# Kernel optimization log

Measured on AMD Instinct MI355X. Metric: run time of the kernel, lower is better.

Reference implementation:

```python
import jax, jax.numpy as jnp
import numpy as np

N = 100000
E = 1000000
IN_C = 128
HID = 128
HEADS = 4
DH = HID // HEADS
L = 2
RWSE_DIM = 16
WALK_LEN = 16
NPAIRS = 200000
EPS = 1e-5


def setup_inputs() -> dict:
    key = jax.random.key(0)
    ks = jax.random.split(key, 20)
    x = jax.random.normal(ks[0], (N, IN_C), dtype=jnp.float32)
    rw_diag = jax.random.uniform(ks[1], (N, WALK_LEN), dtype=jnp.float32)
    edge_index = jax.random.randint(ks[2], (2, E), 0, N, dtype=jnp.int32)
    src = jax.random.randint(ks[3], (NPAIRS,), 0, N, dtype=jnp.int32)
    dst = jax.random.randint(ks[4], (NPAIRS,), 0, N, dtype=jnp.int32)
    s = 0.05
    W_rwse = jax.random.normal(ks[5], (WALK_LEN, RWSE_DIM), dtype=jnp.float32) * s
    b_rwse = jnp.zeros((RWSE_DIM,), dtype=jnp.float32)
    W_in = jax.random.normal(ks[6], (IN_C + RWSE_DIM, HID), dtype=jnp.float32) * s
    b_in = jnp.zeros((HID,), dtype=jnp.float32)
    Wq = jax.random.normal(ks[7], (L, HID, HID), dtype=jnp.float32) * s
    bq = jnp.zeros((L, HID), dtype=jnp.float32)
    Wk = jax.random.normal(ks[8], (L, HID, HID), dtype=jnp.float32) * s
    bk = jnp.zeros((L, HID), dtype=jnp.float32)
    Wv = jax.random.normal(ks[9], (L, HID, HID), dtype=jnp.float32) * s
    bv = jnp.zeros((L, HID), dtype=jnp.float32)
    Ws = jax.random.normal(ks[10], (L, HID, HID), dtype=jnp.float32) * s
    bs = jnp.zeros((L, HID), dtype=jnp.float32)
    ln_g = jnp.ones((L, HID), dtype=jnp.float32)
    ln_b = jnp.zeros((L, HID), dtype=jnp.float32)
    return {"x": x, "rw_diag": rw_diag, "edge_index": edge_index, "src": src,
            "dst": dst, "W_rwse": W_rwse, "b_rwse": b_rwse, "W_in": W_in,
            "b_in": b_in, "Wq": Wq, "bq": bq, "Wk": Wk, "bk": bk, "Wv": Wv,
            "bv": bv, "Ws": Ws, "bs": bs, "ln_g": ln_g, "ln_b": ln_b}


def reference(x, rw_diag, edge_index, src, dst, W_rwse, b_rwse, W_in, b_in,
              Wq, bq, Wk, bk, Wv, bv, Ws, bs, ln_g, ln_b):
    row = edge_index[0]  # message source j
    col = edge_index[1]  # message target i
    # RWSE projection + input projection
    pe = rw_diag @ W_rwse + b_rwse                      # [N, rwse_dim]
    h = jnp.concatenate([x, pe], axis=-1) @ W_in + b_in  # [N, HID]
    scale = 1.0 / jnp.sqrt(jnp.float32(DH))
    for l in range(L):
        q = (h @ Wq[l] + bq[l]).reshape(N, HEADS, DH)
        k = (h @ Wk[l] + bk[l]).reshape(N, HEADS, DH)
        v = (h @ Wv[l] + bv[l]).reshape(N, HEADS, DH)
        # per-edge attention scores (gather)
        score = jnp.einsum('ehd,ehd->eh', q[col], k[row]) * scale  # [E, H]
        # segment softmax over incoming edges of each target node
        m = jax.ops.segment_max(score, col, num_segments=N)   # [N, H]
        ex = jnp.exp(score - m[col])
        z = jax.ops.segment_sum(ex, col, num_segments=N)      # [N, H]
        alpha = ex / z[col]                                   # [E, H]
        agg = jax.ops.segment_sum(alpha[:, :, None] * v[row], col,
                                  num_segments=N).reshape(N, HID)
        conv = agg + h @ Ws[l] + bs[l]  # root/skip linear (PyG lin_skip)
        # residual + LayerNorm + ReLU
        y = h + conv
        mu = jnp.mean(y, axis=-1, keepdims=True)
        var = jnp.mean(jnp.square(y - mu), axis=-1, keepdims=True)
        h = jax.nn.relu(ln_g[l] * (y - mu) / jnp.sqrt(var + EPS) + ln_b[l])
    logits = jnp.sum(h[src] * h[dst], axis=-1)  # [NPAIRS]
    return jax.nn.sigmoid(logits)
```

## Files before the change

### kernel.cpp

```cpp
#include <hip/hip_runtime.h>
#include <hip/hip_bf16.h>
#include <cstdint>


#define NN      100000
#define EE      1000000
#define RWSEC   16
#define WALKC   16
#define NPAIRSC 200000
#define BSH     9
#define BKT     ((NN + 511) >> BSH)

typedef unsigned int       u32;
typedef unsigned short     u16;
typedef unsigned char      u8;
typedef __attribute__((ext_vector_type(8))) short    short8;
typedef __attribute__((ext_vector_type(4))) float    f32x4;
typedef __attribute__((ext_vector_type(2))) _Float16 h2;

__device__ __forceinline__ float bflo(u32 u){ return __uint_as_float(u << 16); }
__device__ __forceinline__ float bfhi(u32 u){ return __uint_as_float(u & 0xffff0000u); }
__device__ __forceinline__ u16 f2bf(float f){
    u32 u = __float_as_uint(f);
    u += 0x7fffu + ((u >> 16) & 1u);
    return (u16)(u >> 16);
}
__device__ __forceinline__ u32 pack2(float a, float b){
    return (u32)f2bf(a) | ((u32)f2bf(b) << 16);
}

#if defined(__has_builtin)
#if __has_builtin(__builtin_amdgcn_cvt_pk_f32_fp8) && __has_builtin(__builtin_amdgcn_cvt_pk_fp8_f32)
#define HWFP8 1
#endif
#if __has_builtin(__builtin_amdgcn_sdot4)
#define USE_SDOT4 1
#endif
#if __has_builtin(__builtin_amdgcn_cvt_pk_f16_fp8)
#define HWF16FP8 1
#endif
#endif

#ifndef HWFP8
__device__ __forceinline__ float fp8dec1(u32 b){
    u32 s = (b >> 7) & 1u, e = (b >> 3) & 15u, m = b & 7u;
    float mag = e ? __uint_as_float(((e + 120u) << 23) | (m << 20))
                  : (float)m * 0.001953125f;
    return s ? -mag : mag;
}
__device__ __forceinline__ u32 fp8enc1(float f){
    u32 u = __float_as_uint(f); u32 s = (u >> 31) << 7; float a = fabsf(f);
    if (a >= 448.f) return s | 0x7Eu;
    u32 ua = __float_as_uint(a);
    ua += 0x7FFFFu + ((ua >> 20) & 1u);
    int e = (int)(ua >> 23) - 127 + 7;
    if (e <= 0){ int m = (int)rintf(a * 512.f); return s | (u32)m; }
    u32 m = (ua >> 20) & 7u;
    return s | ((u32)e << 3) | m;
}
#endif

__device__ __forceinline__ void fp8x4_dec(u32 w4, float& f0, float& f1, float& f2, float& f3){
#ifdef HWFP8
    auto lo = __builtin_amdgcn_cvt_pk_f32_fp8((int)w4, false);
    auto hi = __builtin_amdgcn_cvt_pk_f32_fp8((int)w4, true);
    f0 = lo[0]; f1 = lo[1]; f2 = hi[0]; f3 = hi[1];
#else
    f0 = fp8dec1(w4 & 255u); f1 = fp8dec1((w4 >> 8) & 255u);
    f2 = fp8dec1((w4 >> 16) & 255u); f3 = fp8dec1(w4 >> 24);
#endif
}
__device__ __forceinline__ u32 fp8x4_enc(float f0, float f1, float f2, float f3){
#ifdef HWFP8
    u32 t = (u32)__builtin_amdgcn_cvt_pk_fp8_f32(f0, f1, 0, false);
    return (u32)__builtin_amdgcn_cvt_pk_fp8_f32(f2, f3, (int)t, true);
#else
    return fp8enc1(f0) | (fp8enc1(f1) << 8) | (fp8enc1(f2) << 16) | (fp8enc1(f3) << 24);
#endif
}
__device__ __forceinline__ void fp8x4_to_h2(u32 w, h2& lo, h2& hi){
#ifdef HWF16FP8
    lo = __builtin_bit_cast(h2, __builtin_amdgcn_cvt_pk_f16_fp8((int)w, false));
    hi = __builtin_bit_cast(h2, __builtin_amdgcn_cvt_pk_f16_fp8((int)w, true));
#else
    float f0, f1, f2, f3;
    fp8x4_dec(w, f0, f1, f2, f3);
    lo = __builtin_bit_cast(h2, __builtin_amdgcn_cvt_pkrtz(f0, f1));
    hi = __builtin_bit_cast(h2, __builtin_amdgcn_cvt_pkrtz(f2, f3));
#endif
}

#define QSCALE    48.0f
#define DESCALE2  1.10693e-4f

__device__ __forceinline__ int i8q(float f){
    float c = fminf(fmaxf(f * QSCALE, -127.f), 127.f);
    return (int)rintf(c);
}
__device__ __forceinline__ u32 i8x4_enc(float f0, float f1, float f2, float f3){
    return (u32)(i8q(f0) & 255) | ((u32)(i8q(f1) & 255) << 8)
         | ((u32)(i8q(f2) & 255) << 16) | ((u32)(i8q(f3) & 255) << 24);
}
__device__ __forceinline__ float sb(u32 w, int i){
    return (float)(int)(signed char)((w >> (i * 8)) & 255u);
}

__global__ __launch_bounds__(256) void winprep_kernel(const float* __restrict__ Win,
                                                      u16* __restrict__ Winb){
    int t = blockIdx.x * 256 + threadIdx.x;
    if (t >= 8 * 5 * 64) return;
    int lane = t & 63, fi = t >> 6;
    int nt = fi / 5, kk = fi - nt * 5;
    int col = nt * 16 + (lane & 15);
    int k0  = kk * 32 + (lane >> 4) * 8;
    u16* dst = Winb + (size_t)fi * 512 + lane * 8;
    #pragma unroll
    for (int e = 0; e < 8; ++e){
        int k = k0 + e;
        dst[e] = (k < 144) ? f2bf(Win[(size_t)k * 128 + col]) : (u16)0;
    }
}

__global__ __launch_bounds__(512, 8) void inproj_mfma(const float* __restrict__ x,
        const float* __restrict__ rw, const float* __restrict__ Wr,
        const float* __restrict__ br,
        const u16* __restrict__ Winb, const float* __restrict__ bin,
        u16* __restrict__ hb){
    __shared__ u16   hs[64 * 168];
    __shared__ float rws[64 * 16];
    int tid = threadIdx.x;
    int n0  = blockIdx.x * 64;

    #pragma unroll
    for (int i = 0; i < 4; ++i){
        int g   = i * 512 + tid;
        int row = g >> 5, c4 = g & 31;
        float4 f = make_float4(0.f, 0.f, 0.f, 0.f);
        if (n0 + row < NN)
            f = *reinterpret_cast<const float4*>(x + (size_t)(n0 + row) * 128 + c4 * 4);
        *reinterpret_cast<uint2*>((char*)hs + row * 336 + c4 * 8)
            = make_uint2(pack2(f.x, f.y), pack2(f.z, f.w));
    }
    if (tid < 256){
        int row = tid >> 2, c4 = tid & 3;
        float4 f = make_float4(0.f, 0.f, 0.f, 0.f);
        if (n0 + row < NN)
            f = *reinterpret_cast<const float4*>(rw + (size_t)(n0 + row) * 16 + c4 * 4);
        *reinterpret_cast<float4*>(&rws[row * 16 + c4 * 4]) = f;
    }
    __syncthreads();
    if (tid < 256){
        int row = tid >> 2, j0 = (tid & 3) * 4;
        float p0 = br[j0], p1 = br[j0 + 1], p2 = br[j0 + 2], p3 = br[j0 + 3];
        #pragma unroll
        for (int w = 0; w < 16; ++w){
            float r = rws[row * 16 + w];
            const float4 wv = *reinterpret_cast<const float4*>(Wr + w * 16 + j0);
            p0 = fmaf(r, wv.x, p0); p1 = fmaf(r, wv.y, p1);
            p2 = fmaf(r, wv.z, p2); p3 = fmaf(r, wv.w, p3);
        }
        *reinterpret_cast<uint2*>((char*)hs + row * 336 + 256 + (tid & 3) * 8)
            = make_uint2(pack2(p0, p1), pack2(p2, p3));
        *reinterpret_cast<uint2*>((char*)hs + row * 336 + 288 + (tid & 3) * 8)
            = make_uint2(0u, 0u);
    }
    __syncthreads();

    int l = tid & 63, w = tid >> 6;
    int r16 = l & 15, kq = l >> 4;
    const short8* wfrag = reinterpret_cast<const short8*>(Winb) + (size_t)(w * 5) * 64;
    f32x4 acc[4];
    #pragma unroll
    for (int rg = 0; rg < 4; ++rg) acc[rg] = (f32x4){0.f, 0.f, 0.f, 0.f};
    for (int kk = 0; kk < 5; ++kk){
        short8 wf = wfrag[kk * 64 + l];
        #pragma unroll
        for (int rg = 0; rg < 4; ++rg){
            int row = rg * 16 + r16;
            short8 hf = *reinterpret_cast<const short8*>(
                (const char*)hs + row * 336 + kk * 64 + kq * 16);
            acc[rg] = __builtin_amdgcn_mfma_f32_16x16x32_bf16(wf, hf, acc[rg], 0, 0, 0);
        }
    }
    float4 bv = *reinterpret_cast<const float4*>(bin + w * 16 + kq * 4);
    #pragma unroll
    for (int rg = 0; rg < 4; ++rg){
        int row = rg * 16 + r16;
        if (n0 + row < NN){
            u32 lo = pack2(acc[rg][0] + bv.x, acc[rg][1] + bv.y);
            u32 hi = pack2(acc[rg][2] + bv.z, acc[rg][3] + bv.w);
            *reinterpret_cast<uint2*>(hb + (size_t)(n0 + row) * 128 + w * 16 + kq * 4)
                = make_uint2(lo, hi);
        }
    }
}

__global__ __launch_bounds__(256) void bhist_kernel(const int* __restrict__ col,
                                                    int* __restrict__ bcnt){
    __shared__ int h[BKT];
    int tid = threadIdx.x;
    for (int i = tid; i < BKT; i += 256) h[i] = 0;
    __syncthreads();
    for (int e = blockIdx.x * 256 + tid; e < EE; e += gridDim.x * 256)
        atomicAdd(&h[col[e] >> BSH], 1);
    __syncthreads();
    for (int i = tid; i < BKT; i += 256)
        if (h[i]) atomicAdd(&bcnt[i], h[i]);
}

__global__ __launch_bounds__(256) void bscan_kernel(const int* __restrict__ bcnt,
                                                    int* __restrict__ bstart,
                                                    int* __restrict__ bwork){
    __shared__ int lds[256];
    int tid = threadIdx.x;
    int v = (tid < BKT) ? bcnt[tid] : 0;
    lds[tid] = v;
    __syncthreads();
    for (int off = 1; off < 256; off <<= 1){
        int y = (tid >= off) ? lds[tid - off] : 0;
        __syncthreads();
        lds[tid] += y;
        __syncthreads();
    }
    if (tid < BKT){ int p = lds[tid] - v; bstart[tid] = p; bwork[tid] = p; }
}

__global__ __launch_bounds__(256) void bpart_kernel(const int* __restrict__ ei,
                                                    int* __restrict__ bwork,
                                                    u32* __restrict__ bkt){
    __shared__ int cnt_[BKT], base_[BKT], rnk_[BKT];
    int tid = threadIdx.x;
    for (int i = tid; i < BKT; i += 256){ cnt_[i] = 0; rnk_[i] = 0; }
    __syncthreads();
    for (int e = blockIdx.x * 256 + tid; e < EE; e += gridDim.x * 256)
        atomicAdd(&cnt_[ei[EE + e] >> BSH], 1);
    __syncthreads();
    for (int i = tid; i < BKT; i += 256)
        base_[i] = cnt_[i] ? atomicAdd(&bwork[i], cnt_[i]) : 0;
    __syncthreads();
    for (int e = blockIdx.x * 256 + tid; e < EE; e += gridDim.x * 256){
        int c = ei[EE + e], b = c >> BSH;
        int p = base_[b] + atomicAdd(&rnk_[b], 1);
        bkt[p] = ((u32)ei[e] << BSH) | (u32)(c & 511);
    }
}

__global__ __launch_bounds__(256) void bcsr_kernel(const int* __restrict__ bstart,
                                                   const int* __restrict__ bcnt,
                                                   const u32* __restrict__ bkt,
                                                   int* __restrict__ offs,
                                                   int* __restrict__ deg,
                                                   int* __restrict__ ebuf){
    __shared__ int dcnt[512];
    __shared__ int pref[512];
    __shared__ int psum[256];
    int b   = blockIdx.x;
    int tid = threadIdx.x;
    int n0  = b << BSH;
    int nb  = NN - n0 < 512 ? NN - n0 : 512;
    int e0  = bstart[b];
    int ec  = bcnt[b];
    dcnt[tid] = 0; dcnt[tid + 256] = 0;
    __syncthreads();
    for (int i = tid; i < ec; i += 256)
        atomicAdd(&dcnt[bkt[e0 + i] & 511u], 1);
    __syncthreads();
    int s0 = dcnt[2 * tid], s1 = dcnt[2 * tid + 1];
    psum[tid] = s0 + s1;
    __syncthreads();
    for (int off = 1; off < 256; off <<= 1){
        int y = (tid >= off) ? psum[tid - off] : 0;
        __syncthreads();
        psum[tid] += y;
        __syncthreads();
    }
    int exq = psum[tid] - (s0 + s1);
    pref[2 * tid]     = exq;
    pref[2 * tid + 1] = exq + s0;
    __syncthreads();
    for (int i = tid; i < nb; i += 256){
        offs[n0 + i] = e0 + pref[i];
        deg[n0 + i]  = dcnt[i];
    }
    __syncthreads();
    for (int i = tid; i < ec; i += 256){
        u32 rc = bkt[e0 + i];
        int p = atomicAdd(&pref[rc & 511u], 1);
        ebuf[e0 + p] = (int)((rc >> BSH) << 8);
    }
}

__global__ __launch_bounds__(256) void dhist_kernel(const int* __restrict__ deg,
                                                    int* __restrict__ dh){
    __shared__ int h[256];
    int tid = threadIdx.x;
    h[tid] = 0;
    __syncthreads();
    for (int i = blockIdx.x * 256 + tid; i < NN; i += gridDim.x * 256){
        int d = deg[i]; d = d > 255 ? 255 : d;
        atomicAdd(&h[d], 1);
    }
    __syncthreads();
    if (h[tid]) atomicAdd(&dh[tid], h[tid]);
}

__global__ __launch_bounds__(256) void dscan_kernel(const int* __restrict__ dh,
                                                    int* __restrict__ dcur){
    __shared__ int lds[256];
    int tid = threadIdx.x;
    int v = dh[tid];
    lds[tid] = v;
    __syncthreads();
    for (int off = 1; off < 256; off <<= 1){
        int y = (tid >= off) ? lds[tid - off] : 0;
        __syncthreads();
        lds[tid] += y;
        __syncthreads();
    }
    dcur[tid] = lds[tid] - v;
}

__global__ __launch_bounds__(256) void dfill_kernel(const int* __restrict__ deg,
                                                    int* __restrict__ dcur,
                                                    int* __restrict__ perm){
    __shared__ int cnt_[256], base_[256], rnk_[256];
    int tid = threadIdx.x;
    cnt_[tid] = 0; rnk_[tid] = 0;
    __syncthreads();
    for (int i = blockIdx.x * 256 + tid; i < NN; i += gridDim.x * 256){
        int d = deg[i]; d = d > 255 ? 255 : d;
        atomicAdd(&cnt_[d], 1);
    }
    __syncthreads();
    base_[tid] = cnt_[tid] ? atomicAdd(&dcur[tid], cnt_[tid]) : 0;
    __syncthreads();
    for (int i = blockIdx.x * 256 + tid; i < NN; i += gridDim.x * 256){
        int d = deg[i]; d = d > 255 ? 255 : d;
        int p = base_[d] + atomicAdd(&rnk_[d], 1);
        perm[p] = i;
    }
}

__global__ __launch_bounds__(256) void wprep_kernel(const float* __restrict__ Wq,
        const float* __restrict__ Wk, const float* __restrict__ Wv,
        const float* __restrict__ Ws, u16* __restrict__ Wb2){
    int t = blockIdx.x * 256 + threadIdx.x;
    if (t >= 2 * 128 * 64) return;
    int lane = t & 63, fi = (t >> 6) & 127, l = t >> 13;
    int gnt = fi >> 2, kk = fi & 3;
    int m = gnt >> 3;
    int col = (gnt * 16 + (lane & 15)) & 127;
    const float* W = (m == 0 ? Wq : m == 1 ? Wk : m == 2 ? Wv : Ws) + (size_t)l * 16384;
    int k0 = kk * 32 + (lane >> 4) * 8;
    u16* dst = Wb2 + ((size_t)l * 128 + fi) * 512 + lane * 8;
    #pragma unroll
    for (int e = 0; e < 8; ++e) dst[e] = f2bf(W[(size_t)(k0 + e) * 128 + col]);
}

__global__ __launch_bounds__(256) void gemm4_mfma(const u16* __restrict__ hb,
        const u16* __restrict__ Wb2,
        const float* __restrict__ bq, const float* __restrict__ bk,
        const float* __restrict__ bv, const float* __restrict__ bs,
        u8* __restrict__ qb, u8* __restrict__ kvb, u16* __restrict__ hsb){
    __shared__ u16 hs[64 * 128];
    __shared__ u16 ob[4][64 * 128];
    int tid = threadIdx.x;
    int n0  = blockIdx.x * 64;
    #pragma unroll
    for (int i = 0; i < 4; ++i){
        int c = i * 256 + tid;
        int row = c >> 4, cb = (c & 15) * 16;
        uint4 v = make_uint4(0u, 0u, 0u, 0u);
        if (n0 + row < NN)
            v = *reinterpret_cast<const uint4*>(hb + (size_t)(n0 + row) * 128 + cb / 2);
        *reinterpret_cast<uint4*>((char*)hs + row * 256 + (cb ^ ((row & 7) << 4))) = v;
    }
    __syncthreads();
    int l = tid & 63, w = tid >> 6;
    int r16 = l & 15, kq = l >> 4;
    short8 ha[4][4];
    #pragma unroll
    for (int rg = 0; rg < 4; ++rg)
        #pragma unroll
        for (int kk = 0; kk < 4; ++kk){
            int row = rg * 16 + r16;
            int byt = (kk * 64 + kq * 16) ^ ((row & 7) << 4);
            ha[rg][kk] = *reinterpret_cast<const short8*>((const char*)hs + row * 256 + byt);
        }
    const float* bp = w == 0 ? bq : w == 1 ? bk : w == 2 ? bv : bs;
    const short8* wfrag = reinterpret_cast<const short8*>(Wb2) + (size_t)(w * 8) * 4 * 64;
    u16* myob = &ob[w][0];
    #pragma unroll
    for (int nt = 0; nt < 8; ++nt){
        f32x4 acc[4];
        #pragma unroll
        for (int rg = 0; rg < 4; ++rg) acc[rg] = (f32x4){0.f, 0.f, 0.f, 0.f};
        #pragma unroll
        for (int kk = 0; kk < 4; ++kk){
            short8 wf = wfrag[(nt * 4 + kk) * 64 + l];
            #pragma unroll
            for (int rg = 0; rg < 4; ++rg)
                acc[rg] = __builtin_amdgcn_mfma_f32_16x16x32_bf16(wf, ha[rg][kk], acc[rg], 0, 0, 0);
        }
        float4 bvv = *reinterpret_cast<const float4*>(bp + nt * 16 + kq * 4);
        #pragma unroll
        for (int rg = 0; rg < 4; ++rg){
            int row = rg * 16 + r16;
            int cb  = (nt * 32 + kq * 8) ^ ((row & 7) << 4);
            float a0 = acc[rg][0] + bvv.x, a1 = acc[rg][1] + bvv.y;
            float a2 = acc[rg][2] + bvv.z, a3 = acc[rg][3] + bvv.w;
            if (w == 3){
                uint2 hval = *reinterpret_cast<const uint2*>((const char*)hs + row * 256 + cb);
                a0 += bflo(hval.x); a1 += bfhi(hval.x);
                a2 += bflo(hval.y); a3 += bfhi(hval.y);
            }
            *reinterpret_cast<uint2*>((char*)myob + row * 256 + cb)
                = make_uint2(pack2(a0, a1), pack2(a2, a3));
        }
    }
    asm volatile("s_waitcnt lgkmcnt(0)" ::: "memory");
    if (w == 1 || w == 2){
        int off = (w == 2) ? 8 : 0;
        #pragma unroll
        for (int i = 0; i < 16; ++i){
            int row = i * 4 + kq;
            int cb  = r16 * 16;
            uint4 v = *reinterpret_cast<const uint4*>(
                (char*)myob + row * 256 + (cb ^ ((row & 7) << 4)));
            if (n0 + row < NN){
                u32 A, B;
#ifdef USE_SDOT4
                if (w == 1){
                    A = i8x4_enc(bflo(v.x), bfhi(v.x), bflo(v.y), bfhi(v.y));
                    B = i8x4_enc(bflo(v.z), bfhi(v.z), bflo(v.w), bfhi(v.w));
                } else
#endif
                {
                    A = fp8x4_enc(bflo(v.x), bfhi(v.x), bflo(v.y), bfhi(v.y));
                    B = fp8x4_enc(bflo(v.z), bfhi(v.z), bflo(v.w), bfhi(v.w));
                }
                *reinterpret_cast<uint2*>((char*)kvb + (size_t)(n0 + row) * 256
                                          + r16 * 16 + off) = make_uint2(A, B);
            }
        }
    } else if (w == 0){
        #pragma unroll
        for (int i = 0; i < 16; ++i){
            int row = i * 4 + kq;
            int cb  = r16 * 16;
            uint4 v = *reinterpret_cast<const uint4*>(
                (char*)myob + row * 256 + (cb ^ ((row & 7) << 4)));
            if (n0 + row < NN){
#ifdef USE_SDOT4
                u32 A = i8x4_enc(bflo(v.x), bfhi(v.x), bflo(v.y), bfhi(v.y));
                u32 B = i8x4_enc(bflo(v.z), bfhi(v.z), bflo(v.w), bfhi(v.w));
                *reinterpret_cast<uint2*>(qb + (size_t)(n0 + row) * 128 + cb / 2)
                    = make_uint2(A, B);
#else
                *reinterpret_cast<uint4*>((u16*)qb + (size_t)(n0 + row) * 128 + cb / 2) = v;
#endif
            }
        }
    } else {
        #pragma unroll
        for (int i = 0; i < 16; ++i){
            int row = i * 4 + kq;
            int cb  = r16 * 16;
            uint4 v = *reinterpret_cast<const uint4*>(
                (char*)myob + row * 256 + (cb ^ ((row & 7) << 4)));
            if (n0 + row < NN)
                *reinterpret_cast<uint4*>(hsb + (size_t)(n0 + row) * 128 + cb / 2) = v;
        }
    }
}

__global__ __launch_bounds__(256) void attn_kernel(u16* __restrict__ hb,
        const u8* __restrict__ qb, const u8* __restrict__ kvb,
        const u16* __restrict__ hsb,
        const int* __restrict__ offs, const int* __restrict__ deg,
        const int* __restrict__ ebuf, const int* __restrict__ perm,
        const float* __restrict__ gw, const float* __restrict__ bta){
    int tid = threadIdx.x;
    int gq  = tid & 15;
    int n   = perm[blockIdx.x * 16 + (tid >> 4)];
#ifdef USE_SDOT4
    uint2 qu = *reinterpret_cast<const uint2*>(qb + (size_t)n * 128 + gq * 8);
    int qi0 = (int)qu.x, qi1 = (int)qu.y;
#else
    const float scale = 0.17677669529663687f;
    uint4 qu = *reinterpret_cast<const uint4*>((const u16*)qb + (size_t)n * 128 + gq * 8);
    float q0 = bflo(qu.x) * scale, q1 = bfhi(qu.x) * scale;
    float q2 = bflo(qu.y) * scale, q3 = bfhi(qu.y) * scale;
    float q4 = bflo(qu.z) * scale, q5 = bfhi(qu.z) * scale;
    float q6 = bflo(qu.w) * scale, q7 = bfhi(qu.w) * scale;
#endif
    int beg = offs[n], cnt = deg[n];
    float z = 0.f;
    h2 acc01 = (h2)0, acc23 = (h2)0, acc45 = (h2)0, acc67 = (h2)0;
    const u8* kvg = kvb + gq * 16;

#ifdef USE_SDOT4
    #define SCORE(kv)                                                                 \
        float s;                                                                      \
        {   int si = __builtin_amdgcn_sdot4((int)kv.x, qi0, 0, false);                \
            si = __builtin_amdgcn_sdot4((int)kv.y, qi1, si, false);                   \
            s = (float)si * DESCALE2; }
#else
    #define SCORE(kv)                                                                 \
        float s;                                                                      \
        {   s = q0*sb(kv.x,0) + q1*sb(kv.x,1) + q2*sb(kv.x,2) + q3*sb(kv.x,3)         \
              + q4*sb(kv.y,0) + q5*sb(kv.y,1) + q6*sb(kv.y,2) + q7*sb(kv.y,3);        \
            s *= (1.4426950408889634f / QSCALE); }
#endif

    #define CONSUME(kv)                                                               \
    {   SCORE(kv);                                                                    \
        s += __shfl_xor(s, 1); s += __shfl_xor(s, 2);                                 \
        float ex = exp2f(s);                                                          \
        h2 v01, v23, v45, v67;                                                        \
        fp8x4_to_h2(kv.z, v01, v23);                                                  \
        fp8x4_to_h2(kv.w, v45, v67);                                                  \
        z += ex;                                                                      \
        _Float16 exh = (_Float16)ex;                                                  \
        h2 exv = {exh, exh};                                                          \
        acc01 = __builtin_elementwise_fma(exv, v01, acc01);                           \
        acc23 = __builtin_elementwise_fma(exv, v23, acc23);                           \
        acc45 = __builtin_elementwise_fma(exv, v45, acc45);                           \
        acc67 = __builtin_elementwise_fma(exv, v67, acc67);  }

    #define GATHER(off_) (*reinterpret_cast<const uint4*>(kvg + (size_t)(u32)(off_)))

    if (cnt > 0){
        uint4 kv = GATHER(ebuf[beg]);
        for (int t = 1; t < cnt; ++t){
            uint4 nk = GATHER(ebuf[beg + t]);
            CONSUME(kv);
            kv = nk;
        }
        CONSUME(kv);
    }
    #undef CONSUME
    #undef GATHER
    #undef SCORE

    float rz = (cnt > 0) ? 1.f / z : 0.f;
    float a0 = (float)acc01[0], a1 = (float)acc01[1];
    float a2 = (float)acc23[0], a3 = (float)acc23[1];
    float a4 = (float)acc45[0], a5 = (float)acc45[1];
    float a6 = (float)acc67[0], a7 = (float)acc67[1];

    size_t p = (size_t)n * 128 + gq * 8;
    uint4 hu = *reinterpret_cast<const uint4*>(hsb + p);
    float y0 = bflo(hu.x) + a0 * rz, y1 = bfhi(hu.x) + a1 * rz;
    float y2 = bflo(hu.y) + a2 * rz, y3 = bfhi(hu.y) + a3 * rz;
    float y4 = bflo(hu.z) + a4 * rz, y5 = bfhi(hu.z) + a5 * rz;
    float y6 = bflo(hu.w) + a6 * rz, y7 = bfhi(hu.w) + a7 * rz;
    float sum = y0 + y1 + y2 + y3 + y4 + y5 + y6 + y7;
    float sq  = y0*y0 + y1*y1 + y2*y2 + y3*y3 + y4*y4 + y5*y5 + y6*y6 + y7*y7;
    #pragma unroll
    for (int m = 1; m < 16; m <<= 1){
        sum += __shfl_xor(sum, m);
        sq  += __shfl_xor(sq,  m);
    }
    float mu  = sum * (1.f / 128.f);
    float var = sq * (1.f / 128.f) - mu * mu;
    var = var < 0.f ? 0.f : var;
    float inv = rsqrtf(var + 1e-5f);
    int c = gq * 8;
    float4 gm0 = *reinterpret_cast<const float4*>(gw + c);
    float4 gm1 = *reinterpret_cast<const float4*>(gw + c + 4);
    float4 bt0 = *reinterpret_cast<const float4*>(bta + c);
    float4 bt1 = *reinterpret_cast<const float4*>(bta + c + 4);
    float o0 = fmaf(gm0.x * (y0 - mu), inv, bt0.x);
    float o1 = fmaf(gm0.y * (y1 - mu), inv, bt0.y);
    float o2 = fmaf(gm0.z * (y2 - mu), inv, bt0.z);
    float o3 = fmaf(gm0.w * (y3 - mu), inv, bt0.w);
    float o4 = fmaf(gm1.x * (y4 - mu), inv, bt1.x);
    float o5 = fmaf(gm1.y * (y5 - mu), inv, bt1.y);
    float o6 = fmaf(gm1.z * (y6 - mu), inv, bt1.z);
    float o7 = fmaf(gm1.w * (y7 - mu), inv, bt1.w);
    o0 = o0 > 0.f ? o0 : 0.f;  o1 = o1 > 0.f ? o1 : 0.f;
    o2 = o2 > 0.f ? o2 : 0.f;  o3 = o3 > 0.f ? o3 : 0.f;
    o4 = o4 > 0.f ? o4 : 0.f;  o5 = o5 > 0.f ? o5 : 0.f;
    o6 = o6 > 0.f ? o6 : 0.f;  o7 = o7 > 0.f ? o7 : 0.f;
    *reinterpret_cast<uint4*>(hb + p) = make_uint4(
        pack2(o0, o1), pack2(o2, o3), pack2(o4, o5), pack2(o6, o7));
}

__global__ __launch_bounds__(256) void pair_kernel(const u16* __restrict__ hb,
                                                   const int* __restrict__ src,
                                                   const int* __restrict__ dst,
                                                   float* __restrict__ out){
    int tid = threadIdx.x;
    int pid = blockIdx.x * 16 + (tid >> 4);
    int sub = tid & 15;
    int s = src[pid], d = dst[pid];
    uint4 a = *reinterpret_cast<const uint4*>(hb + (size_t)s * 128 + sub * 8);
    uint4 b = *reinterpret_cast<const uint4*>(hb + (size_t)d * 128 + sub * 8);
    float dot = bflo(a.x) * bflo(b.x) + bfhi(a.x) * bfhi(b.x)
              + bflo(a.y) * bflo(b.y) + bfhi(a.y) * bfhi(b.y)
              + bflo(a.z) * bflo(b.z) + bfhi(a.z) * bfhi(b.z)
              + bflo(a.w) * bflo(b.w) + bfhi(a.w) * bfhi(b.w);
    dot += __shfl_xor(dot, 1); dot += __shfl_xor(dot, 2);
    dot += __shfl_xor(dot, 4); dot += __shfl_xor(dot, 8);
    if (sub == 0) out[pid] = 1.f / (1.f + __expf(-dot));
}

extern "C" void kernel_launch(void* const* d_in, const int* in_sizes, int n_in,
                              void* d_out, int out_size, void* d_ws, size_t ws_size,
                              hipStream_t stream){
    const float* x      = (const float*)d_in[0];
    const float* rw     = (const float*)d_in[1];
    const int*   ei     = (const int*)  d_in[2];
    const int*   src    = (const int*)  d_in[3];
    const int*   dst    = (const int*)  d_in[4];
    const float* W_rwse = (const float*)d_in[5];
    const float* b_rwse = (const float*)d_in[6];
    const float* W_in   = (const float*)d_in[7];
    const float* b_in   = (const float*)d_in[8];
    const float* Wq     = (const float*)d_in[9];
    const float* bq     = (const float*)d_in[10];
    const float* Wk     = (const float*)d_in[11];
    const float* bk     = (const float*)d_in[12];
    const float* Wv     = (const float*)d_in[13];
    const float* bv     = (const float*)d_in[14];
    const float* Wsk    = (const float*)d_in[15];
    const float* bsk    = (const float*)d_in[16];
    const float* ln_g   = (const float*)d_in[17];
    const float* ln_b   = (const float*)d_in[18];
    float* out = (float*)d_out;

    char* p = (char*)d_ws;
    auto carve = [&](size_t bytes) -> char* {
        char* r = p; p += (bytes + 255) & ~(size_t)255; return r;
    };
    u16*   hb    = (u16*) carve((size_t)NN * 128 * 2);
    u8*    qb    = (u8*)  carve((size_t)NN * 128 * 2);
    u8*    kvb   = (u8*)  carve((size_t)NN * 256);
    u16*   hsb   = (u16*) carve((size_t)NN * 128 * 2);
    int*   offs  = (int*) carve((size_t)NN * 4);
    int*   deg   = (int*) carve((size_t)NN * 4);
    int*   ebuf  = (int*) carve((size_t)EE * 4);
    u32*   bkt   = (u32*) carve((size_t)EE * 4);
    int*   bcnt  = (int*) carve((size_t)BKT * 4);
    int*   bstart= (int*) carve((size_t)BKT * 4);
    int*   bwork = (int*) carve((size_t)BKT * 4);
    int*   perm  = (int*) carve((size_t)NN * 4);
    int*   dh    = (int*) carve((size_t)256 * 4);
    int*   dcur  = (int*) carve((size_t)256 * 4);
    u16*   Wb2   = (u16*) carve((size_t)2 * 128 * 512 * 2);
    u16*   Winb  = (u16*) carve((size_t)8 * 5 * 512 * 2);

    hipMemsetAsync(bcnt, 0, (size_t)BKT * 4, stream);
    hipMemsetAsync(dh, 0, (size_t)256 * 4, stream);

    winprep_kernel<<<10, 256, 0, stream>>>(W_in, Winb);
    wprep_kernel<<<64, 256, 0, stream>>>(Wq, Wk, Wv, Wsk, Wb2);
    inproj_mfma<<<(NN + 63) / 64, 512, 0, stream>>>(x, rw, W_rwse, b_rwse,
                                                    Winb, b_in, hb);
    bhist_kernel<<<512, 256, 0, stream>>>(ei + EE, bcnt);
    bscan_kernel<<<1, 256, 0, stream>>>(bcnt, bstart, bwork);
    bpart_kernel<<<512, 256, 0, stream>>>(ei, bwork, bkt);
    bcsr_kernel<<<BKT, 256, 0, stream>>>(bstart, bcnt, bkt, offs, deg, ebuf);
    dhist_kernel<<<256, 256, 0, stream>>>(deg, dh);
    dscan_kernel<<<1, 256, 0, stream>>>(dh, dcur);
    dfill_kernel<<<256, 256, 0, stream>>>(deg, dcur, perm);

    for (int l = 0; l < 2; ++l){
        gemm4_mfma<<<(NN + 63) / 64, 256, 0, stream>>>(hb, Wb2 + (size_t)l * 65536,
            bq + l * 128, bk + l * 128, bv + l * 128, bsk + l * 128,
            qb, kvb, hsb);
        attn_kernel<<<NN / 16, 256, 0, stream>>>(hb, qb, kvb, hsb,
            offs, deg, ebuf, perm, ln_g + l * 128, ln_b + l * 128);
    }
    pair_kernel<<<NPAIRSC / 16, 256, 0, stream>>>(hb, src, dst, out);
}
```

Baseline: 299.7 us.

## Drop GEMM output LDS staging, stream A fragments, raise occupancy hint

The projection GEMM kernel no longer stages its outputs in a 64KB shared buffer before re-encoding and storing. Each wave now writes bias-added results straight to global memory as bf16 or fp8 from its MFMA accumulators. The A fragments are read from LDS inside the k-loop instead of being held in registers, and launch bounds now request 8 blocks per SM. These changes cut LDS use and register pressure to allow higher occupancy, at the cost of narrower, less coalesced 4-8 byte global stores and repeated LDS reads. The score computation in the attention kernel also switches from a scaled byte extraction to an fp8 decode helper, which drops the QSCALE division.

```diff
diff --git a/kernel.cpp b/kernel.cpp
--- a/kernel.cpp
+++ b/kernel.cpp
@@ -357,13 +357,12 @@
     for (int e = 0; e < 8; ++e) dst[e] = f2bf(W[(size_t)(k0 + e) * 128 + col]);
 }
 
-__global__ __launch_bounds__(256) void gemm4_mfma(const u16* __restrict__ hb,
+__global__ __launch_bounds__(256, 8) void gemm4_mfma(const u16* __restrict__ hb,
         const u16* __restrict__ Wb2,
         const float* __restrict__ bq, const float* __restrict__ bk,
         const float* __restrict__ bv, const float* __restrict__ bs,
         u8* __restrict__ qb, u8* __restrict__ kvb, u16* __restrict__ hsb){
     __shared__ u16 hs[64 * 128];
-    __shared__ u16 ob[4][64 * 128];
     int tid = threadIdx.x;
     int n0  = blockIdx.x * 64;
     #pragma unroll
@@ -378,19 +377,8 @@
     __syncthreads();
     int l = tid & 63, w = tid >> 6;
     int r16 = l & 15, kq = l >> 4;
-    short8 ha[4][4];
-    #pragma unroll
-    for (int rg = 0; rg < 4; ++rg)
-        #pragma unroll
-        for (int kk = 0; kk < 4; ++kk){
-            int row = rg * 16 + r16;
-            int byt = (kk * 64 + kq * 16) ^ ((row & 7) << 4);
-            ha[rg][kk] = *reinterpret_cast<const short8*>((const char*)hs + row * 256 + byt);
-        }
     const float* bp = w == 0 ? bq : w == 1 ? bk : w == 2 ? bv : bs;
     const short8* wfrag = reinterpret_cast<const short8*>(Wb2) + (size_t)(w * 8) * 4 * 64;
-    u16* myob = &ob[w][0];
-    #pragma unroll
     for (int nt = 0; nt < 8; ++nt){
         f32x4 acc[4];
         #pragma unroll
@@ -399,77 +387,50 @@
         for (int kk = 0; kk < 4; ++kk){
             short8 wf = wfrag[(nt * 4 + kk) * 64 + l];
             #pragma unroll
-            for (int rg = 0; rg < 4; ++rg)
-                acc[rg] = __builtin_amdgcn_mfma_f32_16x16x32_bf16(wf, ha[rg][kk], acc[rg], 0, 0, 0);
+            for (int rg = 0; rg < 4; ++rg){
+                int row = rg * 16 + r16;
+                int byt = (kk * 64 + kq * 16) ^ ((row & 7) << 4);
+                short8 hf = *reinterpret_cast<const short8*>(
+                    (const char*)hs + row * 256 + byt);
+                acc[rg] = __builtin_amdgcn_mfma_f32_16x16x32_bf16(wf, hf, acc[rg], 0, 0, 0);
+            }
         }
         float4 bvv = *reinterpret_cast<const float4*>(bp + nt * 16 + kq * 4);
         #pragma unroll
         for (int rg = 0; rg < 4; ++rg){
             int row = rg * 16 + r16;
-            int cb  = (nt * 32 + kq * 8) ^ ((row & 7) << 4);
+            if (n0 + row >= NN) continue;
             float a0 = acc[rg][0] + bvv.x, a1 = acc[rg][1] + bvv.y;
             float a2 = acc[rg][2] + bvv.z, a3 = acc[rg][3] + bvv.w;
-            if (w == 3){
+            int col = nt * 16 + kq * 4;
+            if (w == 0){
+#ifdef USE_SDOT4
+                *reinterpret_cast<u32*>(qb + (size_t)(n0 + row) * 128 + col)
+                    = i8x4_enc(a0, a1, a2, a3);
+#else
+                *reinterpret_cast<uint2*>((u16*)qb + (size_t)(n0 + row) * 128 + col)
+                    = make_uint2(pack2(a0, a1), pack2(a2, a3));
+#endif
+            } else if (w == 1){
+                u32 pk;
+#ifdef USE_SDOT4
+                pk = i8x4_enc(a0, a1, a2, a3);
+#else
+                pk = fp8x4_enc(a0, a1, a2, a3);
+#endif
+                *reinterpret_cast<u32*>(kvb + (size_t)(n0 + row) * 256
+                    + (col >> 3) * 16 + (col & 7)) = pk;
+            } else if (w == 2){
+                *reinterpret_cast<u32*>(kvb + (size_t)(n0 + row) * 256
+                    + (col >> 3) * 16 + 8 + (col & 7)) = fp8x4_enc(a0, a1, a2, a3);
+            } else {
+                int cb = (col * 2) ^ ((row & 7) << 4);
                 uint2 hval = *reinterpret_cast<const uint2*>((const char*)hs + row * 256 + cb);
                 a0 += bflo(hval.x); a1 += bfhi(hval.x);
                 a2 += bflo(hval.y); a3 += bfhi(hval.y);
+                *reinterpret_cast<uint2*>(hsb + (size_t)(n0 + row) * 128 + col)
+                    = make_uint2(pack2(a0, a1), pack2(a2, a3));
             }
-            *reinterpret_cast<uint2*>((char*)myob + row * 256 + cb)
-                = make_uint2(pack2(a0, a1), pack2(a2, a3));
-        }
-    }
-    asm volatile("s_waitcnt lgkmcnt(0)" ::: "memory");
-    if (w == 1 || w == 2){
-        int off = (w == 2) ? 8 : 0;
-        #pragma unroll
-        for (int i = 0; i < 16; ++i){
-            int row = i * 4 + kq;
-            int cb  = r16 * 16;
-            uint4 v = *reinterpret_cast<const uint4*>(
-                (char*)myob + row * 256 + (cb ^ ((row & 7) << 4)));
-            if (n0 + row < NN){
-                u32 A, B;
-#ifdef USE_SDOT4
-                if (w == 1){
-                    A = i8x4_enc(bflo(v.x), bfhi(v.x), bflo(v.y), bfhi(v.y));
-                    B = i8x4_enc(bflo(v.z), bfhi(v.z), bflo(v.w), bfhi(v.w));
-                } else
-#endif
-                {
-                    A = fp8x4_enc(bflo(v.x), bfhi(v.x), bflo(v.y), bfhi(v.y));
-                    B = fp8x4_enc(bflo(v.z), bfhi(v.z), bflo(v.w), bfhi(v.w));
-                }
-                *reinterpret_cast<uint2*>((char*)kvb + (size_t)(n0 + row) * 256
-                                          + r16 * 16 + off) = make_uint2(A, B);
-            }
-        }
-    } else if (w == 0){
-        #pragma unroll
-        for (int i = 0; i < 16; ++i){
-            int row = i * 4 + kq;
-            int cb  = r16 * 16;
-            uint4 v = *reinterpret_cast<const uint4*>(
-                (char*)myob + row * 256 + (cb ^ ((row & 7) << 4)));
-            if (n0 + row < NN){
-#ifdef USE_SDOT4
-                u32 A = i8x4_enc(bflo(v.x), bfhi(v.x), bflo(v.y), bfhi(v.y));
-                u32 B = i8x4_enc(bflo(v.z), bfhi(v.z), bflo(v.w), bfhi(v.w));
-                *reinterpret_cast<uint2*>(qb + (size_t)(n0 + row) * 128 + cb / 2)
-                    = make_uint2(A, B);
-#else
-                *reinterpret_cast<uint4*>((u16*)qb + (size_t)(n0 + row) * 128 + cb / 2) = v;
-#endif
-            }
-        }
-    } else {
-        #pragma unroll
-        for (int i = 0; i < 16; ++i){
-            int row = i * 4 + kq;
-            int cb  = r16 * 16;
-            uint4 v = *reinterpret_cast<const uint4*>(
-                (char*)myob + row * 256 + (cb ^ ((row & 7) << 4)));
-            if (n0 + row < NN)
-                *reinterpret_cast<uint4*>(hsb + (size_t)(n0 + row) * 128 + cb / 2) = v;
         }
     }
 }
@@ -508,9 +469,10 @@
 #else
     #define SCORE(kv)                                                                 \
         float s;                                                                      \
-        {   s = q0*sb(kv.x,0) + q1*sb(kv.x,1) + q2*sb(kv.x,2) + q3*sb(kv.x,3)         \
-              + q4*sb(kv.y,0) + q5*sb(kv.y,1) + q6*sb(kv.y,2) + q7*sb(kv.y,3);        \
-            s *= (1.4426950408889634f / QSCALE); }
+        {   float k0,k1,k2,k3,k4,k5,k6,k7;                                            \
+            fp8x4_dec(kv.x, k0, k1, k2, k3); fp8x4_dec(kv.y, k4, k5, k6, k7);         \
+            s = q0*k0 + q1*k1 + q2*k2 + q3*k3 + q4*k4 + q5*k5 + q6*k6 + q7*k7;        \
+            s *= 1.4426950408889634f; }
 #endif
 
     #define CONSUME(kv)                                                               \
```

After: 540.8 us. 1.8x slower.

## Split gemm4 work across 8 waves and decode fp8 keys with packed conversion

Applied to the files above, without the earlier changes.

The fused Q/K/V/skip GEMM kernel now launches 512 threads per block, with two waves per output matrix, each handling half of the 64 rows. This halves per-wave A-fragment registers and accumulators and allows more waves in flight, at the cost of each weight fragment being loaded by two waves. Separately, the fp8 key score path in attention now decodes four bytes at once through a helper instead of per-byte extraction, and drops the QSCALE division from the exp2 scaling factor.

```diff
diff --git a/kernel.cpp b/kernel.cpp
--- a/kernel.cpp
+++ b/kernel.cpp
@@ -357,7 +357,7 @@
     for (int e = 0; e < 8; ++e) dst[e] = f2bf(W[(size_t)(k0 + e) * 128 + col]);
 }
 
-__global__ __launch_bounds__(256) void gemm4_mfma(const u16* __restrict__ hb,
+__global__ __launch_bounds__(512, 4) void gemm4_mfma(const u16* __restrict__ hb,
         const u16* __restrict__ Wb2,
         const float* __restrict__ bq, const float* __restrict__ bk,
         const float* __restrict__ bv, const float* __restrict__ bs,
@@ -367,8 +367,8 @@
     int tid = threadIdx.x;
     int n0  = blockIdx.x * 64;
     #pragma unroll
-    for (int i = 0; i < 4; ++i){
-        int c = i * 256 + tid;
+    for (int i = 0; i < 2; ++i){
+        int c = i * 512 + tid;
         int row = c >> 4, cb = (c & 15) * 16;
         uint4 v = make_uint4(0u, 0u, 0u, 0u);
         if (n0 + row < NN)
@@ -377,39 +377,39 @@
     }
     __syncthreads();
     int l = tid & 63, w = tid >> 6;
+    int m = w >> 1, rh = w & 1;
     int r16 = l & 15, kq = l >> 4;
-    short8 ha[4][4];
-    #pragma unroll
-    for (int rg = 0; rg < 4; ++rg)
+    short8 ha[2][4];
+    #pragma unroll
+    for (int g = 0; g < 2; ++g)
         #pragma unroll
         for (int kk = 0; kk < 4; ++kk){
-            int row = rg * 16 + r16;
+            int row = (rh * 2 + g) * 16 + r16;
             int byt = (kk * 64 + kq * 16) ^ ((row & 7) << 4);
-            ha[rg][kk] = *reinterpret_cast<const short8*>((const char*)hs + row * 256 + byt);
-        }
-    const float* bp = w == 0 ? bq : w == 1 ? bk : w == 2 ? bv : bs;
-    const short8* wfrag = reinterpret_cast<const short8*>(Wb2) + (size_t)(w * 8) * 4 * 64;
-    u16* myob = &ob[w][0];
+            ha[g][kk] = *reinterpret_cast<const short8*>((const char*)hs + row * 256 + byt);
+        }
+    const float* bp = m == 0 ? bq : m == 1 ? bk : m == 2 ? bv : bs;
+    const short8* wfrag = reinterpret_cast<const short8*>(Wb2) + (size_t)(m * 8) * 4 * 64;
+    u16* myob = &ob[m][0];
     #pragma unroll
     for (int nt = 0; nt < 8; ++nt){
-        f32x4 acc[4];
-        #pragma unroll
-        for (int rg = 0; rg < 4; ++rg) acc[rg] = (f32x4){0.f, 0.f, 0.f, 0.f};
+        f32x4 acc[2];
+        acc[0] = (f32x4){0.f, 0.f, 0.f, 0.f};
+        acc[1] = (f32x4){0.f, 0.f, 0.f, 0.f};
         #pragma unroll
         for (int kk = 0; kk < 4; ++kk){
             short8 wf = wfrag[(nt * 4 + kk) * 64 + l];
-            #pragma unroll
-            for (int rg = 0; rg < 4; ++rg)
-                acc[rg] = __builtin_amdgcn_mfma_f32_16x16x32_bf16(wf, ha[rg][kk], acc[rg], 0, 0, 0);
+            acc[0] = __builtin_amdgcn_mfma_f32_16x16x32_bf16(wf, ha[0][kk], acc[0], 0, 0, 0);
+            acc[1] = __builtin_amdgcn_mfma_f32_16x16x32_bf16(wf, ha[1][kk], acc[1], 0, 0, 0);
         }
         float4 bvv = *reinterpret_cast<const float4*>(bp + nt * 16 + kq * 4);
         #pragma unroll
-        for (int rg = 0; rg < 4; ++rg){
-            int row = rg * 16 + r16;
+        for (int g = 0; g < 2; ++g){
+            int row = (rh * 2 + g) * 16 + r16;
             int cb  = (nt * 32 + kq * 8) ^ ((row & 7) << 4);
-            float a0 = acc[rg][0] + bvv.x, a1 = acc[rg][1] + bvv.y;
-            float a2 = acc[rg][2] + bvv.z, a3 = acc[rg][3] + bvv.w;
-            if (w == 3){
+            float a0 = acc[g][0] + bvv.x, a1 = acc[g][1] + bvv.y;
+            float a2 = acc[g][2] + bvv.z, a3 = acc[g][3] + bvv.w;
+            if (m == 3){
                 uint2 hval = *reinterpret_cast<const uint2*>((const char*)hs + row * 256 + cb);
                 a0 += bflo(hval.x); a1 += bfhi(hval.x);
                 a2 += bflo(hval.y); a3 += bfhi(hval.y);
@@ -419,18 +419,18 @@
         }
     }
     asm volatile("s_waitcnt lgkmcnt(0)" ::: "memory");
-    if (w == 1 || w == 2){
-        int off = (w == 2) ? 8 : 0;
-        #pragma unroll
-        for (int i = 0; i < 16; ++i){
-            int row = i * 4 + kq;
+    if (m == 1 || m == 2){
+        int off = (m == 2) ? 8 : 0;
+        #pragma unroll
+        for (int i = 0; i < 8; ++i){
+            int row = rh * 32 + i * 4 + kq;
             int cb  = r16 * 16;
             uint4 v = *reinterpret_cast<const uint4*>(
                 (char*)myob + row * 256 + (cb ^ ((row & 7) << 4)));
             if (n0 + row < NN){
                 u32 A, B;
 #ifdef USE_SDOT4
-                if (w == 1){
+                if (m == 1){
                     A = i8x4_enc(bflo(v.x), bfhi(v.x), bflo(v.y), bfhi(v.y));
                     B = i8x4_enc(bflo(v.z), bfhi(v.z), bflo(v.w), bfhi(v.w));
                 } else
@@ -443,10 +443,10 @@
                                           + r16 * 16 + off) = make_uint2(A, B);
             }
         }
-    } else if (w == 0){
-        #pragma unroll
-        for (int i = 0; i < 16; ++i){
-            int row = i * 4 + kq;
+    } else if (m == 0){
+        #pragma unroll
+        for (int i = 0; i < 8; ++i){
+            int row = rh * 32 + i * 4 + kq;
             int cb  = r16 * 16;
             uint4 v = *reinterpret_cast<const uint4*>(
                 (char*)myob + row * 256 + (cb ^ ((row & 7) << 4)));
@@ -463,8 +463,8 @@
         }
     } else {
         #pragma unroll
-        for (int i = 0; i < 16; ++i){
-            int row = i * 4 + kq;
+        for (int i = 0; i < 8; ++i){
+            int row = rh * 32 + i * 4 + kq;
             int cb  = r16 * 16;
             uint4 v = *reinterpret_cast<const uint4*>(
                 (char*)myob + row * 256 + (cb ^ ((row & 7) << 4)));
@@ -508,9 +508,10 @@
 #else
     #define SCORE(kv)                                                                 \
         float s;                                                                      \
-        {   s = q0*sb(kv.x,0) + q1*sb(kv.x,1) + q2*sb(kv.x,2) + q3*sb(kv.x,3)         \
-              + q4*sb(kv.y,0) + q5*sb(kv.y,1) + q6*sb(kv.y,2) + q7*sb(kv.y,3);        \
-            s *= (1.4426950408889634f / QSCALE); }
+        {   float k0,k1,k2,k3,k4,k5,k6,k7;                                            \
+            fp8x4_dec(kv.x, k0, k1, k2, k3); fp8x4_dec(kv.y, k4, k5, k6, k7);         \
+            s = q0*k0 + q1*k1 + q2*k2 + q3*k3 + q4*k4 + q5*k5 + q6*k6 + q7*k7;        \
+            s *= 1.4426950408889634f; }
 #endif
 
     #define CONSUME(kv)                                                               \
@@ -667,7 +668,7 @@
     dfill_kernel<<<256, 256, 0, stream>>>(deg, dcur, perm);
 
     for (int l = 0; l < 2; ++l){
-        gemm4_mfma<<<(NN + 63) / 64, 256, 0, stream>>>(hb, Wb2 + (size_t)l * 65536,
+        gemm4_mfma<<<(NN + 63) / 64, 512, 0, stream>>>(hb, Wb2 + (size_t)l * 65536,
             bq + l * 128, bk + l * 128, bv + l * 128, bsk + l * 128,
             qb, kvb, hsb);
         attn_kernel<<<NN / 16, 256, 0, stream>>>(hb, qb, kvb, hsb,
```

Result: faster. 279.7 us (-6.7%).
